# Kernel optimization log

Measured on AMD Instinct MI355X. Metric: run time of the kernel, lower is better.

## Reference

```python
import jax, jax.numpy as jnp
import numpy as np


def setup_inputs() -> dict:
    key = jax.random.key(0)
    k1, k2, k3, k4 = jax.random.split(key, 4)
    B, S, D_IN, D_OUT = 32, 4096, 256, 256
    input = jax.random.normal(k1, (B, S, D_IN), dtype=jnp.float32)
    data_mask = jax.random.randint(k2, (B, S), 0, 2).astype(jnp.bool_)
    W = jax.random.normal(k3, (D_IN, D_OUT), dtype=jnp.float32) * (1.0 / np.sqrt(D_IN))
    b = jax.random.normal(k4, (D_OUT,), dtype=jnp.float32) * 0.01
    return {"input": input, "data_mask": data_mask, "W": W, "b": b}


def reference(input, data_mask, W, b):
    # ObjWise: gather non-pad tokens, apply op (Linear+ReLU), scatter back,
    # pad positions filled with zeros. Since the op is per-token, this equals
    # applying the op everywhere and zeroing pad positions.
    # input: (B, S, D_in), data_mask: (B, S)
    y = jax.nn.relu(jnp.einsum("bsd,de->bse", input, W) + b)  # (B, S, D_out)
    return jnp.where(data_mask[..., None], y, jnp.zeros((), dtype=y.dtype))
```

## Files before the change

### kernel.cpp

```cpp
#include <hip/hip_runtime.h>
#include <hip/hip_bf16.h>


typedef __attribute__((ext_vector_type(8))) short bf16x8;
typedef __attribute__((ext_vector_type(4))) float f32x4;

#define KD 256
#define ND 256

static __device__ __forceinline__ unsigned short f2bf(float f) {
  union { float f; unsigned u; } x; x.f = f;
  unsigned r = x.u + 0x7FFFu + ((x.u >> 16) & 1u);
  return (unsigned short)(r >> 16);
}

__global__ void detect_mask_kernel(const unsigned int* __restrict__ mw,
                                   int* __restrict__ flag) {
  __shared__ int s;
  if (threadIdx.x == 0) s = 0;
  __syncthreads();
  unsigned w = mw[threadIdx.x];
  int f = 0;
  if (w == 0x3F800000u) f = 2;
  else if (w > 1u) f = 1;
  if (f) atomicOr(&s, f);
  __syncthreads();
  if (threadIdx.x == 0) *flag = (s & 2) ? 2 : (s & 1);
}

static __device__ __forceinline__ bool mrow(const void* mp, int flag, int row) {
  if (flag == 2) return ((const float*)mp)[row] != 0.0f;
  if (flag == 1) return ((const unsigned char*)mp)[row] != 0;
  return ((const int*)mp)[row] != 0;
}

__global__ void prep_w_kernel(const float* __restrict__ W,
                              unsigned short* __restrict__ wf) {
  int k = blockIdx.x;
  int n = threadIdx.x;
  float v = W[k * ND + n];
  int nb = n >> 4;
  int kb = k >> 5;
  int lane = (n & 15) | (((k >> 3) & 3) << 4);
  int e = k & 7;
  wf[(((nb << 3) | kb) << 9) + (lane << 3) + e] = f2bf(v);
}

__global__ __launch_bounds__(256) void objwise_gemm(
    const float* __restrict__ A, const void* __restrict__ mask,
    const unsigned short* __restrict__ wf, const float* __restrict__ bias,
    float* __restrict__ out, const int* __restrict__ flagp) {
  const int flag = *flagp;
  const int tid  = threadIdx.x;
  const int wave = tid >> 6;
  const int lane = tid & 63;
  const int rb = blockIdx.x * 64 + (wave >> 1) * 32;
  const int cb = (wave & 1) * 128;

  const int r0   = rb + (lane & 15);
  const int r1   = r0 + 16;
  const int koff = (lane >> 4) << 3;

  const bool m0 = mrow(mask, flag, r0);
  const bool m1 = mrow(mask, flag, r1);

  const float* a0p = A + (size_t)r0 * KD + koff;
  const float* a1p = A + (size_t)r1 * KD + koff;
  const unsigned short* wfl = wf + ((size_t)(cb >> 4) << 12) + (lane << 3);

  f32x4 acc[2][8];
#pragma unroll
  for (int i = 0; i < 8; ++i) {
    acc[0][i] = (f32x4){0.f, 0.f, 0.f, 0.f};
    acc[1][i] = (f32x4){0.f, 0.f, 0.f, 0.f};
  }

#pragma unroll 2
  for (int kb = 0; kb < 8; ++kb) {
    bf16x8 a0 = (bf16x8){0,0,0,0,0,0,0,0};
    bf16x8 a1 = (bf16x8){0,0,0,0,0,0,0,0};
    if (m0) {
      f32x4 x = *(const f32x4*)(a0p + kb * 32);
      f32x4 y = *(const f32x4*)(a0p + kb * 32 + 4);
      a0[0] = (short)f2bf(x[0]); a0[1] = (short)f2bf(x[1]);
      a0[2] = (short)f2bf(x[2]); a0[3] = (short)f2bf(x[3]);
      a0[4] = (short)f2bf(y[0]); a0[5] = (short)f2bf(y[1]);
      a0[6] = (short)f2bf(y[2]); a0[7] = (short)f2bf(y[3]);
    }
    if (m1) {
      f32x4 x = *(const f32x4*)(a1p + kb * 32);
      f32x4 y = *(const f32x4*)(a1p + kb * 32 + 4);
      a1[0] = (short)f2bf(x[0]); a1[1] = (short)f2bf(x[1]);
      a1[2] = (short)f2bf(x[2]); a1[3] = (short)f2bf(x[3]);
      a1[4] = (short)f2bf(y[0]); a1[5] = (short)f2bf(y[1]);
      a1[6] = (short)f2bf(y[2]); a1[7] = (short)f2bf(y[3]);
    }
#pragma unroll
    for (int n = 0; n < 8; ++n) {
      bf16x8 bfr = *(const bf16x8*)(wfl + ((size_t)n << 12) + (kb << 9));
      acc[0][n] = __builtin_amdgcn_mfma_f32_16x16x32_bf16(a0, bfr, acc[0][n], 0, 0, 0);
      acc[1][n] = __builtin_amdgcn_mfma_f32_16x16x32_bf16(a1, bfr, acc[1][n], 0, 0, 0);
    }
  }

  const int col0 = cb + (lane & 15);
  const int rr   = rb + ((lane >> 4) << 2);

  bool mm0[4], mm1[4];
#pragma unroll
  for (int j = 0; j < 4; ++j) {
    mm0[j] = mrow(mask, flag, rr + j);
    mm1[j] = mrow(mask, flag, rr + 16 + j);
  }
  float bvs[8];
#pragma unroll
  for (int n = 0; n < 8; ++n) bvs[n] = bias[col0 + (n << 4)];

#pragma unroll
  for (int n = 0; n < 8; ++n) {
    const int col = col0 + (n << 4);
#pragma unroll
    for (int j = 0; j < 4; ++j) {
      float v0 = fmaxf(acc[0][n][j] + bvs[n], 0.f);
      out[(size_t)(rr + j) * ND + col] = mm0[j] ? v0 : 0.f;
      float v1 = fmaxf(acc[1][n][j] + bvs[n], 0.f);
      out[(size_t)(rr + 16 + j) * ND + col] = mm1[j] ? v1 : 0.f;
    }
  }
}

extern "C" void kernel_launch(void* const* d_in, const int* in_sizes, int n_in,
                              void* d_out, int out_size, void* d_ws, size_t ws_size,
                              hipStream_t stream) {
  const float* A    = (const float*)d_in[0];
  const void*  mask = d_in[1];
  const float* W    = (const float*)d_in[2];
  const float* bias = (const float*)d_in[3];
  float* out = (float*)d_out;

  int* flag = (int*)d_ws;
  unsigned short* wf = (unsigned short*)((char*)d_ws + 256);

  detect_mask_kernel<<<1, 256, 0, stream>>>((const unsigned int*)mask, flag);
  prep_w_kernel<<<256, 256, 0, stream>>>(W, wf);
  objwise_gemm<<<2048, 256, 0, stream>>>(A, mask, wf, bias, out, flag);
}
```

Baseline: 280.8 us.

## Stage A tile in swizzled LDS as bf16 and merge mask detection into weight prep

Each block now loads its 64x256 fp32 A tile cooperatively with coalesced loads, converts it to bf16, and stores it into XOR-swizzled shared memory. Each wave then computes a 64-column slice across all 64 rows, so the A loads are no longer duplicated across the two column-half waves. The A loads also become unconditional, dropping the per-row mask skip; the mask is applied only at the epilogue. Mask-format detection moves into the weight prep kernel to save one launch, and launch bounds now request 4 blocks per SIMD.

```diff
diff --git a/kernel.cpp b/kernel.cpp
--- a/kernel.cpp
+++ b/kernel.cpp
@@ -4,9 +4,11 @@
 
 typedef __attribute__((ext_vector_type(8))) short bf16x8;
 typedef __attribute__((ext_vector_type(4))) float f32x4;
+typedef __attribute__((ext_vector_type(2))) unsigned int u32x2;
 
 #define KD 256
 #define ND 256
+#define BM 64
 
 static __device__ __forceinline__ unsigned short f2bf(float f) {
   union { float f; unsigned u; } x; x.f = f;
@@ -14,28 +16,16 @@
   return (unsigned short)(r >> 16);
 }
 
-__global__ void detect_mask_kernel(const unsigned int* __restrict__ mw,
-                                   int* __restrict__ flag) {
-  __shared__ int s;
-  if (threadIdx.x == 0) s = 0;
-  __syncthreads();
-  unsigned w = mw[threadIdx.x];
-  int f = 0;
-  if (w == 0x3F800000u) f = 2;
-  else if (w > 1u) f = 1;
-  if (f) atomicOr(&s, f);
-  __syncthreads();
-  if (threadIdx.x == 0) *flag = (s & 2) ? 2 : (s & 1);
-}
-
-static __device__ __forceinline__ bool mrow(const void* mp, int flag, int row) {
+static __device__ __forceinline__ bool mrow(const void* mp, int flag, size_t row) {
   if (flag == 2) return ((const float*)mp)[row] != 0.0f;
   if (flag == 1) return ((const unsigned char*)mp)[row] != 0;
   return ((const int*)mp)[row] != 0;
 }
 
 __global__ void prep_w_kernel(const float* __restrict__ W,
-                              unsigned short* __restrict__ wf) {
+                              unsigned short* __restrict__ wf,
+                              const unsigned int* __restrict__ mw,
+                              int* __restrict__ flag) {
   int k = blockIdx.x;
   int n = threadIdx.x;
   float v = W[k * ND + n];
@@ -44,87 +34,96 @@
   int lane = (n & 15) | (((k >> 3) & 3) << 4);
   int e = k & 7;
   wf[(((nb << 3) | kb) << 9) + (lane << 3) + e] = f2bf(v);
+
+  if (blockIdx.x == 0) {
+    __shared__ int s;
+    if (threadIdx.x == 0) s = 0;
+    __syncthreads();
+    unsigned w = mw[threadIdx.x];
+    int f = 0;
+    if (w == 0x3F800000u) f = 2;
+    else if (w > 1u) f = 1;
+    if (f) atomicOr(&s, f);
+    __syncthreads();
+    if (threadIdx.x == 0) *flag = (s & 2) ? 2 : (s & 1);
+  }
 }
 
-__global__ __launch_bounds__(256) void objwise_gemm(
+__global__ __launch_bounds__(256, 4) void objwise_gemm(
     const float* __restrict__ A, const void* __restrict__ mask,
     const unsigned short* __restrict__ wf, const float* __restrict__ bias,
     float* __restrict__ out, const int* __restrict__ flagp) {
+  __shared__ __align__(16) unsigned char As[BM * KD * 2];
+
   const int flag = *flagp;
   const int tid  = threadIdx.x;
   const int wave = tid >> 6;
   const int lane = tid & 63;
-  const int rb = blockIdx.x * 64 + (wave >> 1) * 32;
-  const int cb = (wave & 1) * 128;
+  const size_t rowbase = (size_t)blockIdx.x * BM;
 
-  const int r0   = rb + (lane & 15);
-  const int r1   = r0 + 16;
-  const int koff = (lane >> 4) << 3;
+  const float* Ab = A + rowbase * KD;
+#pragma unroll
+  for (int i = 0; i < 16; ++i) {
+    f32x4 v = *(const f32x4*)(Ab + i * 1024 + tid * 4);
+    int row  = (i << 2) + (tid >> 6);
+    int colb = (tid << 3) & 511;
+    int baddr = ((row << 9) | colb) ^ ((row & 7) << 4);
+    unsigned p0 = (unsigned)f2bf(v[0]) | ((unsigned)f2bf(v[1]) << 16);
+    unsigned p1 = (unsigned)f2bf(v[2]) | ((unsigned)f2bf(v[3]) << 16);
+    *(u32x2*)(As + baddr) = (u32x2){p0, p1};
+  }
+  __syncthreads();
 
-  const bool m0 = mrow(mask, flag, r0);
-  const bool m1 = mrow(mask, flag, r1);
-
-  const float* a0p = A + (size_t)r0 * KD + koff;
-  const float* a1p = A + (size_t)r1 * KD + koff;
+  const int cb = wave << 6;
   const unsigned short* wfl = wf + ((size_t)(cb >> 4) << 12) + (lane << 3);
 
-  f32x4 acc[2][8];
+  f32x4 acc[4][4];
 #pragma unroll
-  for (int i = 0; i < 8; ++i) {
-    acc[0][i] = (f32x4){0.f, 0.f, 0.f, 0.f};
-    acc[1][i] = (f32x4){0.f, 0.f, 0.f, 0.f};
-  }
+  for (int fr = 0; fr < 4; ++fr)
+#pragma unroll
+    for (int nb = 0; nb < 4; ++nb)
+      acc[fr][nb] = (f32x4){0.f, 0.f, 0.f, 0.f};
+
+  const int arow_l = lane & 15;
+  const int gbyte  = (lane >> 4) << 4;
 
 #pragma unroll 2
   for (int kb = 0; kb < 8; ++kb) {
-    bf16x8 a0 = (bf16x8){0,0,0,0,0,0,0,0};
-    bf16x8 a1 = (bf16x8){0,0,0,0,0,0,0,0};
-    if (m0) {
-      f32x4 x = *(const f32x4*)(a0p + kb * 32);
-      f32x4 y = *(const f32x4*)(a0p + kb * 32 + 4);
-      a0[0] = (short)f2bf(x[0]); a0[1] = (short)f2bf(x[1]);
-      a0[2] = (short)f2bf(x[2]); a0[3] = (short)f2bf(x[3]);
-      a0[4] = (short)f2bf(y[0]); a0[5] = (short)f2bf(y[1]);
-      a0[6] = (short)f2bf(y[2]); a0[7] = (short)f2bf(y[3]);
-    }
-    if (m1) {
-      f32x4 x = *(const f32x4*)(a1p + kb * 32);
-      f32x4 y = *(const f32x4*)(a1p + kb * 32 + 4);
-      a1[0] = (short)f2bf(x[0]); a1[1] = (short)f2bf(x[1]);
-      a1[2] = (short)f2bf(x[2]); a1[3] = (short)f2bf(x[3]);
-      a1[4] = (short)f2bf(y[0]); a1[5] = (short)f2bf(y[1]);
-      a1[6] = (short)f2bf(y[2]); a1[7] = (short)f2bf(y[3]);
+    bf16x8 af[4];
+#pragma unroll
+    for (int fr = 0; fr < 4; ++fr) {
+      int row  = (fr << 4) + arow_l;
+      int addr = (((row << 9) | ((kb << 6) + gbyte))) ^ ((row & 7) << 4);
+      af[fr] = *(const bf16x8*)(As + addr);
     }
 #pragma unroll
-    for (int n = 0; n < 8; ++n) {
-      bf16x8 bfr = *(const bf16x8*)(wfl + ((size_t)n << 12) + (kb << 9));
-      acc[0][n] = __builtin_amdgcn_mfma_f32_16x16x32_bf16(a0, bfr, acc[0][n], 0, 0, 0);
-      acc[1][n] = __builtin_amdgcn_mfma_f32_16x16x32_bf16(a1, bfr, acc[1][n], 0, 0, 0);
+    for (int nb = 0; nb < 4; ++nb) {
+      bf16x8 bfr = *(const bf16x8*)(wfl + ((size_t)nb << 12) + (kb << 9));
+      acc[0][nb] = __builtin_amdgcn_mfma_f32_16x16x32_bf16(af[0], bfr, acc[0][nb], 0, 0, 0);
+      acc[1][nb] = __builtin_amdgcn_mfma_f32_16x16x32_bf16(af[1], bfr, acc[1][nb], 0, 0, 0);
+      acc[2][nb] = __builtin_amdgcn_mfma_f32_16x16x32_bf16(af[2], bfr, acc[2][nb], 0, 0, 0);
+      acc[3][nb] = __builtin_amdgcn_mfma_f32_16x16x32_bf16(af[3], bfr, acc[3][nb], 0, 0, 0);
     }
   }
 
   const int col0 = cb + (lane & 15);
-  const int rr   = rb + ((lane >> 4) << 2);
-
-  bool mm0[4], mm1[4];
+  float bvs[4];
 #pragma unroll
-  for (int j = 0; j < 4; ++j) {
-    mm0[j] = mrow(mask, flag, rr + j);
-    mm1[j] = mrow(mask, flag, rr + 16 + j);
-  }
-  float bvs[8];
-#pragma unroll
-  for (int n = 0; n < 8; ++n) bvs[n] = bias[col0 + (n << 4)];
+  for (int nb = 0; nb < 4; ++nb) bvs[nb] = bias[col0 + (nb << 4)];
 
 #pragma unroll
-  for (int n = 0; n < 8; ++n) {
-    const int col = col0 + (n << 4);
+  for (int fr = 0; fr < 4; ++fr) {
+    const int rl = (fr << 4) + ((lane >> 4) << 2);
 #pragma unroll
     for (int j = 0; j < 4; ++j) {
-      float v0 = fmaxf(acc[0][n][j] + bvs[n], 0.f);
-      out[(size_t)(rr + j) * ND + col] = mm0[j] ? v0 : 0.f;
-      float v1 = fmaxf(acc[1][n][j] + bvs[n], 0.f);
-      out[(size_t)(rr + 16 + j) * ND + col] = mm1[j] ? v1 : 0.f;
+      const size_t grow = rowbase + rl + j;
+      const bool mm = mrow(mask, flag, grow);
+      float* op = out + grow * ND + col0;
+#pragma unroll
+      for (int nb = 0; nb < 4; ++nb) {
+        float v = fmaxf(acc[fr][nb][j] + bvs[nb], 0.f);
+        op[nb << 4] = mm ? v : 0.f;
+      }
     }
   }
 }
@@ -141,7 +140,6 @@
   int* flag = (int*)d_ws;
   unsigned short* wf = (unsigned short*)((char*)d_ws + 256);
 
-  detect_mask_kernel<<<1, 256, 0, stream>>>((const unsigned int*)mask, flag);
-  prep_w_kernel<<<256, 256, 0, stream>>>(W, wf);
+  prep_w_kernel<<<256, 256, 0, stream>>>(W, wf, (const unsigned int*)mask, flag);
   objwise_gemm<<<2048, 256, 0, stream>>>(A, mask, wf, bias, out, flag);
 }
```

New measurement: 258.6 us. -7.9%, faster.
